# Kernel optimization log

Measured on AMD Instinct MI355X. Metric: run time of the kernel, lower is better.

## Reference

```python
import jax, jax.numpy as jnp
import numpy as np

N_NODES = 50000
N_EDGES = 800000
IN_FEATS = 128
HIDDEN = 128
NUM_CLASSES = 47


def setup_inputs() -> dict:
    key = jax.random.key(0)
    k1, k2, k3, k4 = jax.random.split(key, 4)
    features = jax.random.normal(k1, (N_NODES, IN_FEATS), dtype=jnp.float32)
    edge_index = jax.random.randint(k2, (2, N_EDGES), 0, N_NODES, dtype=jnp.int32)
    # Glorot-style init for weights, zeros for bias (DGL GraphConv defaults)
    W1 = jax.random.normal(k3, (IN_FEATS, HIDDEN), dtype=jnp.float32) * (1.0 / np.sqrt(IN_FEATS))
    b1 = jnp.zeros((HIDDEN,), dtype=jnp.float32)
    W2 = jax.random.normal(k4, (HIDDEN, NUM_CLASSES), dtype=jnp.float32) * (1.0 / np.sqrt(HIDDEN))
    b2 = jnp.zeros((NUM_CLASSES,), dtype=jnp.float32)
    return {"features": features, "edge_index": edge_index,
            "W1": W1, "b1": b1, "W2": W2, "b2": b2}


def _graph_conv(x, W, b, src, dst, norm_src, norm_dst, n_nodes):
    # DGL GraphConv, norm='both': D_dst^{-1/2} A D_src^{-1/2} (X W) + b
    h = (x * norm_src[:, None]) @ W            # transform before aggregation
    agg = jax.ops.segment_sum(h[src], dst, num_segments=n_nodes)
    return agg * norm_dst[:, None] + b


def reference(features, edge_index, W1, b1, W2, b2):
    src, dst = edge_index[0], edge_index[1]
    n = features.shape[0]
    ones = jnp.ones((src.shape[0],), dtype=features.dtype)
    deg_out = jax.ops.segment_sum(ones, src, num_segments=n)
    deg_in = jax.ops.segment_sum(ones, dst, num_segments=n)
    norm_src = jax.lax.rsqrt(jnp.clip(deg_out, 1.0))   # d_out^{-1/2}, clamp >= 1
    norm_dst = jax.lax.rsqrt(jnp.clip(deg_in, 1.0))    # d_in^{-1/2}, clamp >= 1

    h = _graph_conv(features, W1, b1, src, dst, norm_src, norm_dst, n)
    h = jax.nn.relu(h)
    out = _graph_conv(h, W2, b2, src, dst, norm_src, norm_dst, n)
    return out
```

## Files before the change

### kernel.cpp

```cpp
#include <hip/hip_runtime.h>
#include <hip/hip_fp16.h>

#define N_NODES 50000
#define N_EDGES 800000
#define IN_F 128
#define HID 128
#define NCLS 47
#define H2S 48
#define W2C 64
#define NCH 196
#define TM 32
#define XTS 40
#define NB 64
#define CHUNK 12500
#define PDW 12500
#define HHALF 6250
#define FQ 3125
#define NHIST 256
#define FG_LDS 20480


struct __align__(8)  h2x2 { __half2 a, b; };
struct __align__(16) h2x4 { __half2 a, b, c, d; };

__global__ __launch_bounds__(512) void hist_kernel(const int* __restrict__ ei,
                                                   unsigned int* __restrict__ Pdst,
                                                   unsigned int* __restrict__ Psrc) {
    __shared__ unsigned int h[HHALF];
    const int t = threadIdx.x;
    const int job = blockIdx.x;
    const bool is_src = job >= NHIST / 2;
    const int half = (job >> 6) & 1;
    const int chunk = job & (NB - 1);
    const int* ids = is_src ? ei : ei + N_EDGES;
    uint2* h2 = (uint2*)h;
    for (int j = t; j < HHALF / 2; j += 512) h2[j] = make_uint2(0u, 0u);
    __syncthreads();
    const int e0 = chunk * CHUNK;
    const int lo = half * HHALF;
    for (int k = t; k < CHUNK; k += 512) {
        int v = ids[e0 + k];
        int rel = (v >> 2) - lo;
        if ((unsigned)rel < HHALF)
            atomicAdd(&h[rel], 1u << ((v & 3) * 8));
    }
    __syncthreads();
    unsigned int* P = (is_src ? Psrc : Pdst) + (size_t)chunk * PDW + lo;
    uint2* P2 = (uint2*)P;
    for (int j = t; j < HHALF / 2; j += 512) P2[j] = h2[j];
}

__global__ __launch_bounds__(256) void reduce_kernel(unsigned int* __restrict__ Pdst,
                                                     const unsigned int* __restrict__ Psrc,
                                                     int* __restrict__ cnt_in,
                                                     float* __restrict__ norm_src,
                                                     float* __restrict__ norm_dst,
                                                     int* __restrict__ chunk_sums) {
    __shared__ int sm[256];
    const int t = threadIdx.x;
    const int j = blockIdx.x * 256 + t;
    int tot = 0;
    if (j < PDW) {
        unsigned int run = 0;
        for (int b = 0; b < NB; ++b) {
            unsigned int v = Pdst[(size_t)b * PDW + j];
            Pdst[(size_t)b * PDW + j] = run;
            run += v;
        }
        int n0 = run & 0xff, n1 = (run >> 8) & 0xff;
        int n2 = (run >> 16) & 0xff, n3 = (run >> 24) & 0xff;
        *(int4*)&cnt_in[4 * j] = make_int4(n0, n1, n2, n3);
        *(float4*)&norm_dst[4 * j] = make_float4(
            rsqrtf(fmaxf((float)n0, 1.0f)), rsqrtf(fmaxf((float)n1, 1.0f)),
            rsqrtf(fmaxf((float)n2, 1.0f)), rsqrtf(fmaxf((float)n3, 1.0f)));
        tot = n0 + n1 + n2 + n3;
        unsigned int rs = 0;
        for (int b = 0; b < NB; ++b) rs += Psrc[(size_t)b * PDW + j];
        int s0 = rs & 0xff, s1 = (rs >> 8) & 0xff;
        int s2 = (rs >> 16) & 0xff, s3 = (rs >> 24) & 0xff;
        *(float4*)&norm_src[4 * j] = make_float4(
            rsqrtf(fmaxf((float)s0, 1.0f)), rsqrtf(fmaxf((float)s1, 1.0f)),
            rsqrtf(fmaxf((float)s2, 1.0f)), rsqrtf(fmaxf((float)s3, 1.0f)));
    }
    sm[t] = tot;
    __syncthreads();
    const int g = t & 63;
    for (int off = 32; off > 0; off >>= 1) {
        if (g < off) sm[t] += sm[t + off];
        __syncthreads();
    }
    if (g == 0) chunk_sums[blockIdx.x * 4 + (t >> 6)] = sm[t];
}

__global__ __launch_bounds__(256) void scan3_kernel(const int* __restrict__ cnt_in,
                                                    const int* __restrict__ chunk_sums,
                                                    int* __restrict__ offsets,
                                                    const float* __restrict__ W2,
                                                    float* __restrict__ W2p) {
    __shared__ int sm[256];
    const int t = threadIdx.x;
    int v = (t < NCH) ? chunk_sums[t] : 0;
    sm[t] = v;
    __syncthreads();
    for (int off = 1; off < 256; off <<= 1) {
        int u = (t >= off) ? sm[t - off] : 0;
        __syncthreads();
        sm[t] += u;
        __syncthreads();
    }
    const int basev = (blockIdx.x == 0) ? 0 : sm[blockIdx.x - 1];
    __syncthreads();
    const int idx = blockIdx.x * 256 + t;
    int c = (idx < N_NODES) ? cnt_in[idx] : 0;
    sm[t] = c;
    __syncthreads();
    for (int off = 1; off < 256; off <<= 1) {
        int u = (t >= off) ? sm[t - off] : 0;
        __syncthreads();
        sm[t] += u;
        __syncthreads();
    }
    if (idx < N_NODES) offsets[idx] = basev + sm[t] - c;
    if (blockIdx.x == 0) {
        if (t == 0) offsets[N_NODES] = N_EDGES;
        for (int i2 = t; i2 < HID * W2C; i2 += 256) {
            int k = i2 >> 6, cc = i2 & 63;
            W2p[i2] = (cc < NCLS) ? W2[k * NCLS + cc] : 0.f;
        }
    }
}

__global__ __launch_bounds__(256) void fill_gemm1_kernel(const int* __restrict__ src,
        const int* __restrict__ dst, const int* __restrict__ offsets,
        const unsigned int* __restrict__ Pdst, int* __restrict__ csr_src,
        const float* __restrict__ X, const float* __restrict__ W1,
        __half* __restrict__ H1h) {
    __shared__ __align__(16) char smem[FG_LDS];
    const int t = threadIdx.x;
    if (blockIdx.x < 4 * NB) {
        unsigned int* cur = (unsigned int*)smem;
        const int quarter = blockIdx.x >> 6;
        const int chunk = blockIdx.x & (NB - 1);
        for (int j = t; j < FQ; j += 256) cur[j] = 0u;
        __syncthreads();
        const unsigned int* base = Pdst + (size_t)chunk * PDW;
        const int e0 = chunk * CHUNK;
        const int lo = quarter * FQ;
        for (int k = t; k < CHUNK; k += 256) {
            int d = dst[e0 + k];
            int rel = (d >> 2) - lo;
            if ((unsigned)rel < FQ) {
                const int sh = (d & 3) * 8;
                unsigned int old = atomicAdd(&cur[rel], 1u << sh);
                unsigned int rank = (old >> sh) & 0xffu;
                unsigned int bh = (base[d >> 2] >> sh) & 0xffu;
                csr_src[offsets[d] + (int)bh + (int)rank] = src[e0 + k];
            }
        }
    } else {
        float* xs = (float*)smem;
        const int row0 = (blockIdx.x - 4 * NB) * TM;
#pragma unroll
        for (int i = 0; i < 4; ++i) {
            int id = t + 256 * i;
            int r = id & 31;
            int q = id >> 5;
            int row = row0 + r;
            float4 v = make_float4(0.f, 0.f, 0.f, 0.f);
            if (row < N_NODES) v = *(const float4*)&X[(size_t)row * IN_F + 4 * q];
            xs[(4 * q + 0) * XTS + r] = v.x;
            xs[(4 * q + 1) * XTS + r] = v.y;
            xs[(4 * q + 2) * XTS + r] = v.z;
            xs[(4 * q + 3) * XTS + r] = v.w;
        }
        __syncthreads();
        const int c = t & 31;
        const int rg = t >> 5;
        float acc[4][4] = {{0.f}};
#pragma unroll 4
        for (int k = 0; k < IN_F; ++k) {
            const float4 w4 = *(const float4*)&W1[k * HID + 4 * c];
            const float4 a4 = *(const float4*)&xs[k * XTS + 4 * rg];
            const float wv[4] = {w4.x, w4.y, w4.z, w4.w};
            const float av[4] = {a4.x, a4.y, a4.z, a4.w};
#pragma unroll
            for (int i = 0; i < 4; ++i)
#pragma unroll
                for (int j = 0; j < 4; ++j)
                    acc[i][j] += av[i] * wv[j];
        }
#pragma unroll
        for (int i = 0; i < 4; ++i) {
            int row = row0 + 4 * rg + i;
            if (row < N_NODES) {
                h2x2 p = {__floats2half2_rn(acc[i][0], acc[i][1]),
                          __floats2half2_rn(acc[i][2], acc[i][3])};
                *(h2x2*)&H1h[(size_t)row * HID + 4 * c] = p;
            }
        }
    }
}

__global__ __launch_bounds__(256) void gather1_kernel(const __half* __restrict__ H1h,
        const int* __restrict__ offsets, const int* __restrict__ csr_src,
        const float* __restrict__ b1, const float* __restrict__ norm_src,
        const float* __restrict__ norm_dst, __half* __restrict__ Hrelu16) {
    const int lane = threadIdx.x & 63;
    const int q = lane >> 4;
    const int fl = lane & 15;
    const int row = blockIdx.x * 4 + (threadIdx.x >> 6);
    const int beg = offsets[row], end = offsets[row + 1];
    float a0 = 0.f, a1 = 0.f, a2 = 0.f, a3 = 0.f;
    float a4 = 0.f, a5 = 0.f, a6 = 0.f, a7 = 0.f;
    for (int base = beg; base < end; base += 64) {
        int idx = 0;
        float nsv = 0.f;
        if (base + lane < end) {
            idx = csr_src[base + lane];
            nsv = norm_src[idx];
        }
        const int cnt = min(end - base, 64);
        for (int j = 0; j < cnt; j += 16) {
            int e0 = j + q, e1 = j + 4 + q, e2 = j + 8 + q, e3 = j + 12 + q;
            int s0 = __shfl(idx, e0);  float n0 = __shfl(nsv, e0);
            int s1 = __shfl(idx, e1);  float n1 = __shfl(nsv, e1);
            int s2 = __shfl(idx, e2);  float n2 = __shfl(nsv, e2);
            int s3 = __shfl(idx, e3);  float n3 = __shfl(nsv, e3);
            h2x4 v0 = *(const h2x4*)&H1h[(size_t)s0 * HID + 8 * fl];
            h2x4 v1 = *(const h2x4*)&H1h[(size_t)s1 * HID + 8 * fl];
            h2x4 v2 = *(const h2x4*)&H1h[(size_t)s2 * HID + 8 * fl];
            h2x4 v3 = *(const h2x4*)&H1h[(size_t)s3 * HID + 8 * fl];
            float2 f;
            f = __half22float2(v0.a); a0 = fmaf(f.x, n0, a0); a1 = fmaf(f.y, n0, a1);
            f = __half22float2(v0.b); a2 = fmaf(f.x, n0, a2); a3 = fmaf(f.y, n0, a3);
            f = __half22float2(v0.c); a4 = fmaf(f.x, n0, a4); a5 = fmaf(f.y, n0, a5);
            f = __half22float2(v0.d); a6 = fmaf(f.x, n0, a6); a7 = fmaf(f.y, n0, a7);
            f = __half22float2(v1.a); a0 = fmaf(f.x, n1, a0); a1 = fmaf(f.y, n1, a1);
            f = __half22float2(v1.b); a2 = fmaf(f.x, n1, a2); a3 = fmaf(f.y, n1, a3);
            f = __half22float2(v1.c); a4 = fmaf(f.x, n1, a4); a5 = fmaf(f.y, n1, a5);
            f = __half22float2(v1.d); a6 = fmaf(f.x, n1, a6); a7 = fmaf(f.y, n1, a7);
            f = __half22float2(v2.a); a0 = fmaf(f.x, n2, a0); a1 = fmaf(f.y, n2, a1);
            f = __half22float2(v2.b); a2 = fmaf(f.x, n2, a2); a3 = fmaf(f.y, n2, a3);
            f = __half22float2(v2.c); a4 = fmaf(f.x, n2, a4); a5 = fmaf(f.y, n2, a5);
            f = __half22float2(v2.d); a6 = fmaf(f.x, n2, a6); a7 = fmaf(f.y, n2, a7);
            f = __half22float2(v3.a); a0 = fmaf(f.x, n3, a0); a1 = fmaf(f.y, n3, a1);
            f = __half22float2(v3.b); a2 = fmaf(f.x, n3, a2); a3 = fmaf(f.y, n3, a3);
            f = __half22float2(v3.c); a4 = fmaf(f.x, n3, a4); a5 = fmaf(f.y, n3, a5);
            f = __half22float2(v3.d); a6 = fmaf(f.x, n3, a6); a7 = fmaf(f.y, n3, a7);
        }
    }
    a0 += __shfl_xor(a0, 16); a1 += __shfl_xor(a1, 16);
    a2 += __shfl_xor(a2, 16); a3 += __shfl_xor(a3, 16);
    a4 += __shfl_xor(a4, 16); a5 += __shfl_xor(a5, 16);
    a6 += __shfl_xor(a6, 16); a7 += __shfl_xor(a7, 16);
    a0 += __shfl_xor(a0, 32); a1 += __shfl_xor(a1, 32);
    a2 += __shfl_xor(a2, 32); a3 += __shfl_xor(a3, 32);
    a4 += __shfl_xor(a4, 32); a5 += __shfl_xor(a5, 32);
    a6 += __shfl_xor(a6, 32); a7 += __shfl_xor(a7, 32);
    if (lane < 16) {
        float nd = norm_dst[row], ns = norm_src[row];
        float4 bA = *(const float4*)&b1[8 * fl];
        float4 bB = *(const float4*)&b1[8 * fl + 4];
        float o0 = fmaxf(fmaf(a0, nd, bA.x), 0.f) * ns;
        float o1 = fmaxf(fmaf(a1, nd, bA.y), 0.f) * ns;
        float o2 = fmaxf(fmaf(a2, nd, bA.z), 0.f) * ns;
        float o3 = fmaxf(fmaf(a3, nd, bA.w), 0.f) * ns;
        float o4 = fmaxf(fmaf(a4, nd, bB.x), 0.f) * ns;
        float o5 = fmaxf(fmaf(a5, nd, bB.y), 0.f) * ns;
        float o6 = fmaxf(fmaf(a6, nd, bB.z), 0.f) * ns;
        float o7 = fmaxf(fmaf(a7, nd, bB.w), 0.f) * ns;
        h2x4 p = {__floats2half2_rn(o0, o1), __floats2half2_rn(o2, o3),
                  __floats2half2_rn(o4, o5), __floats2half2_rn(o6, o7)};
        *(h2x4*)&Hrelu16[(size_t)row * HID + 8 * fl] = p;
    }
}

__global__ __launch_bounds__(128) void gemm2_kernel(const __half* __restrict__ Hrelu16,
                                                    const float* __restrict__ W2p,
                                                    __half* __restrict__ H2h) {
    __shared__ __align__(16) float xs[HID * XTS];
    const int t = threadIdx.x;
    const int row0 = blockIdx.x * TM;
#pragma unroll
    for (int i = 0; i < 4; ++i) {
        int id = t + 128 * i;
        int r = id & 31;
        int g = id >> 5;
        int row = row0 + r;
        h2x4 v{};
        if (row < N_NODES) v = *(const h2x4*)&Hrelu16[(size_t)row * HID + 8 * g];
        float2 f0 = __half22float2(v.a), f1 = __half22float2(v.b);
        float2 f2 = __half22float2(v.c), f3 = __half22float2(v.d);
        xs[(8 * g + 0) * XTS + r] = f0.x;
        xs[(8 * g + 1) * XTS + r] = f0.y;
        xs[(8 * g + 2) * XTS + r] = f1.x;
        xs[(8 * g + 3) * XTS + r] = f1.y;
        xs[(8 * g + 4) * XTS + r] = f2.x;
        xs[(8 * g + 5) * XTS + r] = f2.y;
        xs[(8 * g + 6) * XTS + r] = f3.x;
        xs[(8 * g + 7) * XTS + r] = f3.y;
    }
    __syncthreads();
    const int c = t & 15;
    const int rg = t >> 4;
    float acc[4][4] = {{0.f}};
#pragma unroll 4
    for (int k = 0; k < HID; ++k) {
        const float4 w4 = *(const float4*)&W2p[k * W2C + 4 * c];
        const float4 a4 = *(const float4*)&xs[k * XTS + 4 * rg];
        const float wv[4] = {w4.x, w4.y, w4.z, w4.w};
        const float av[4] = {a4.x, a4.y, a4.z, a4.w};
#pragma unroll
        for (int i = 0; i < 4; ++i)
#pragma unroll
            for (int j = 0; j < 4; ++j)
                acc[i][j] += av[i] * wv[j];
    }
    if (c < 12) {
#pragma unroll
        for (int i = 0; i < 4; ++i) {
            int row = row0 + 4 * rg + i;
            if (row < N_NODES) {
                h2x2 p = {__floats2half2_rn(acc[i][0], acc[i][1]),
                          __floats2half2_rn(acc[i][2], acc[i][3])};
                *(h2x2*)&H2h[(size_t)row * H2S + 4 * c] = p;
            }
        }
    }
}

__global__ __launch_bounds__(256) void gather2_kernel(const __half* __restrict__ H2h,
        const int* __restrict__ offsets, const int* __restrict__ csr_src,
        const float* __restrict__ b2, const float* __restrict__ norm_dst,
        float* __restrict__ out) {
    const int lane = threadIdx.x & 63;
    const int row = blockIdx.x * 4 + (threadIdx.x >> 6);
    const int beg = offsets[row], end = offsets[row + 1];
    const int cl = min(lane, H2S - 1);
    float acc = 0.f;
    for (int base = beg; base < end; base += 64) {
        int idx = 0;
        float wv = 0.f;
        if (base + lane < end) {
            idx = csr_src[base + lane];
            wv = 1.f;
        }
        const int cnt = min(end - base, 64);
        for (int j = 0; j < cnt; j += 4) {
            int s0 = __shfl(idx, j);     float w0 = __shfl(wv, j);
            int s1 = __shfl(idx, j + 1); float w1 = __shfl(wv, j + 1);
            int s2 = __shfl(idx, j + 2); float w2 = __shfl(wv, j + 2);
            int s3 = __shfl(idx, j + 3); float w3 = __shfl(wv, j + 3);
            float f0 = __half2float(H2h[(size_t)s0 * H2S + cl]);
            float f1 = __half2float(H2h[(size_t)s1 * H2S + cl]);
            float f2 = __half2float(H2h[(size_t)s2 * H2S + cl]);
            float f3 = __half2float(H2h[(size_t)s3 * H2S + cl]);
            acc = fmaf(f0, w0, acc);
            acc = fmaf(f1, w1, acc);
            acc = fmaf(f2, w2, acc);
            acc = fmaf(f3, w3, acc);
        }
    }
    if (lane < NCLS) out[(size_t)row * NCLS + lane] = acc * norm_dst[row] + b2[lane];
}

extern "C" void kernel_launch(void* const* d_in, const int* in_sizes, int n_in,
                              void* d_out, int out_size, void* d_ws, size_t ws_size,
                              hipStream_t stream) {
    const float* X  = (const float*)d_in[0];
    const int*   ei = (const int*)d_in[1];
    const float* W1 = (const float*)d_in[2];
    const float* b1 = (const float*)d_in[3];
    const float* W2 = (const float*)d_in[4];
    const float* b2 = (const float*)d_in[5];
    float* out = (float*)d_out;

    const int* src = ei;
    const int* dst = ei + N_EDGES;

    char* w = (char*)d_ws;
    auto alloc = [&](size_t bytes) {
        char* p = w;
        w += (bytes + 255) & ~(size_t)255;
        return p;
    };
    float*  norm_src   = (float*)alloc(N_NODES * 4);
    float*  norm_dst   = (float*)alloc(N_NODES * 4);
    int*    cnt_in     = (int*)alloc(N_NODES * 4);
    int*    offsets    = (int*)alloc((N_NODES + 1) * 4);
    int*    csr_src    = (int*)alloc((size_t)N_EDGES * 4);
    int*    chunk_sums = (int*)alloc(NCH * 4);
    float*  W2p        = (float*)alloc((size_t)HID * W2C * 4);
    __half* H1h        = (__half*)alloc((size_t)N_NODES * HID * 2);
    __half* Hrelu16    = (__half*)alloc((size_t)N_NODES * HID * 2);
    __half* H2h        = (__half*)alloc((size_t)N_NODES * H2S * 2);
    unsigned int* Pdst = (unsigned int*)alloc((size_t)NB * PDW * 4);
    unsigned int* Psrc = (unsigned int*)alloc((size_t)NB * PDW * 4);

    const int gemm_blocks = (N_NODES + TM - 1) / TM;
    hist_kernel<<<NHIST, 512, 0, stream>>>(ei, Pdst, Psrc);
    reduce_kernel<<<(PDW + 255) / 256, 256, 0, stream>>>(Pdst, Psrc, cnt_in,
                                                         norm_src, norm_dst, chunk_sums);
    scan3_kernel<<<NCH, 256, 0, stream>>>(cnt_in, chunk_sums, offsets, W2, W2p);
    fill_gemm1_kernel<<<4 * NB + gemm_blocks, 256, 0, stream>>>(src, dst, offsets,
                                                                Pdst, csr_src,
                                                                X, W1, H1h);
    gather1_kernel<<<N_NODES / 4, 256, 0, stream>>>(H1h, offsets, csr_src, b1,
                                                    norm_src, norm_dst, Hrelu16);
    gemm2_kernel<<<gemm_blocks, 128, 0, stream>>>(Hrelu16, W2p, H2h);
    gather2_kernel<<<N_NODES / 4, 256, 0, stream>>>(H2h, offsets, csr_src, b2,
                                                    norm_dst, out);
}
```

Before: 218.8 us.

## Pad layer-2 hidden rows to 64 halves and gather 8 edges per wave

The layer-2 intermediate rows are padded from 48 to 64 halves so each row is 128 bytes and aligned, and the GEMM epilogue writes all 16 column groups. The second-layer gather now has each wave process 8 edges at once, with 8 lanes per edge each loading 16 bytes (8 halves) through a vector load. Partial sums are combined with xor shuffles before a single lane group writes the output. This replaces the previous scheme of one scalar half load per lane per edge plus index broadcast shuffles, aiming for fewer and wider memory transactions. The cost is extra padding bandwidth on writes and a reduction step at the end.

```diff
diff --git a/kernel.cpp b/kernel.cpp
--- a/kernel.cpp
+++ b/kernel.cpp
@@ -6,7 +6,7 @@
 #define IN_F 128
 #define HID 128
 #define NCLS 47
-#define H2S 48
+#define H2S 64
 #define W2C 64
 #define NCH 196
 #define TM 32
@@ -316,15 +316,13 @@
             for (int j = 0; j < 4; ++j)
                 acc[i][j] += av[i] * wv[j];
     }
-    if (c < 12) {
-#pragma unroll
-        for (int i = 0; i < 4; ++i) {
-            int row = row0 + 4 * rg + i;
-            if (row < N_NODES) {
-                h2x2 p = {__floats2half2_rn(acc[i][0], acc[i][1]),
-                          __floats2half2_rn(acc[i][2], acc[i][3])};
-                *(h2x2*)&H2h[(size_t)row * H2S + 4 * c] = p;
-            }
+#pragma unroll
+    for (int i = 0; i < 4; ++i) {
+        int row = row0 + 4 * rg + i;
+        if (row < N_NODES) {
+            h2x2 p = {__floats2half2_rn(acc[i][0], acc[i][1]),
+                      __floats2half2_rn(acc[i][2], acc[i][3])};
+            *(h2x2*)&H2h[(size_t)row * H2S + 4 * c] = p;
         }
     }
 }
@@ -334,34 +332,41 @@
         const float* __restrict__ b2, const float* __restrict__ norm_dst,
         float* __restrict__ out) {
     const int lane = threadIdx.x & 63;
+    const int es = lane >> 3;
+    const int g = lane & 7;
     const int row = blockIdx.x * 4 + (threadIdx.x >> 6);
     const int beg = offsets[row], end = offsets[row + 1];
-    const int cl = min(lane, H2S - 1);
-    float acc = 0.f;
-    for (int base = beg; base < end; base += 64) {
-        int idx = 0;
-        float wv = 0.f;
-        if (base + lane < end) {
-            idx = csr_src[base + lane];
-            wv = 1.f;
-        }
-        const int cnt = min(end - base, 64);
-        for (int j = 0; j < cnt; j += 4) {
-            int s0 = __shfl(idx, j);     float w0 = __shfl(wv, j);
-            int s1 = __shfl(idx, j + 1); float w1 = __shfl(wv, j + 1);
-            int s2 = __shfl(idx, j + 2); float w2 = __shfl(wv, j + 2);
-            int s3 = __shfl(idx, j + 3); float w3 = __shfl(wv, j + 3);
-            float f0 = __half2float(H2h[(size_t)s0 * H2S + cl]);
-            float f1 = __half2float(H2h[(size_t)s1 * H2S + cl]);
-            float f2 = __half2float(H2h[(size_t)s2 * H2S + cl]);
-            float f3 = __half2float(H2h[(size_t)s3 * H2S + cl]);
-            acc = fmaf(f0, w0, acc);
-            acc = fmaf(f1, w1, acc);
-            acc = fmaf(f2, w2, acc);
-            acc = fmaf(f3, w3, acc);
-        }
-    }
-    if (lane < NCLS) out[(size_t)row * NCLS + lane] = acc * norm_dst[row] + b2[lane];
+    float a0 = 0.f, a1 = 0.f, a2 = 0.f, a3 = 0.f;
+    float a4 = 0.f, a5 = 0.f, a6 = 0.f, a7 = 0.f;
+    for (int base = beg; base < end; base += 8) {
+        int e = base + es;
+        float wv = (e < end) ? 1.f : 0.f;
+        int ec = min(e, end - 1);
+        int s = csr_src[ec];
+        h2x4 v = *(const h2x4*)&H2h[(size_t)s * H2S + 8 * g];
+        float2 f;
+        f = __half22float2(v.a); a0 = fmaf(f.x, wv, a0); a1 = fmaf(f.y, wv, a1);
+        f = __half22float2(v.b); a2 = fmaf(f.x, wv, a2); a3 = fmaf(f.y, wv, a3);
+        f = __half22float2(v.c); a4 = fmaf(f.x, wv, a4); a5 = fmaf(f.y, wv, a5);
+        f = __half22float2(v.d); a6 = fmaf(f.x, wv, a6); a7 = fmaf(f.y, wv, a7);
+    }
+#pragma unroll
+    for (int off = 8; off < 64; off <<= 1) {
+        a0 += __shfl_xor(a0, off); a1 += __shfl_xor(a1, off);
+        a2 += __shfl_xor(a2, off); a3 += __shfl_xor(a3, off);
+        a4 += __shfl_xor(a4, off); a5 += __shfl_xor(a5, off);
+        a6 += __shfl_xor(a6, off); a7 += __shfl_xor(a7, off);
+    }
+    if (es == 0) {
+        const float nd = norm_dst[row];
+        const float av[8] = {a0, a1, a2, a3, a4, a5, a6, a7};
+#pragma unroll
+        for (int i = 0; i < 8; ++i) {
+            int c = 8 * g + i;
+            if (c < NCLS)
+                out[(size_t)row * NCLS + c] = av[i] * nd + b2[c];
+        }
+    }
 }
 
 extern "C" void kernel_launch(void* const* d_in, const int* in_sizes, int n_in,
```

New measurement: 229.4 us. 4.8% more time.
